# Kernel optimization log

Hardware: AMD Instinct MI355X
Metric: run time of the kernel (lower is better)

## Reference

```python
import jax, jax.numpy as jnp
import numpy as np

B, S, DIM, NH = 4, 2048, 2048, 16
HD = DIM // NH  # 128


def setup_inputs() -> dict:
    key = jax.random.key(0)
    ks = jax.random.split(key, 6)
    x = jax.random.normal(ks[0], (B, S, DIM), dtype=jnp.float32)
    wq = jax.random.normal(ks[1], (DIM, DIM), dtype=jnp.float32) * (DIM ** -0.5)
    wk = jax.random.normal(ks[2], (DIM, DIM), dtype=jnp.float32) * (DIM ** -0.5)
    wv = jax.random.normal(ks[3], (DIM, DIM), dtype=jnp.float32) * (DIM ** -0.5)
    wo = jax.random.normal(ks[4], (DIM, DIM), dtype=jnp.float32) * (DIM ** -0.5)
    # RoPE frequencies: theta^{-2i/hd}, angle = pos * freq
    inv_freq = 1.0 / (10000.0 ** (np.arange(0, HD, 2, dtype=np.float32) / HD))  # [HD/2]
    angles = np.arange(S, dtype=np.float32)[:, None] * inv_freq[None, :]  # [S, HD/2]
    freqs_cos = jnp.asarray(np.cos(angles))
    freqs_sin = jnp.asarray(np.sin(angles))
    # causal mask, additive [S, S]
    mask = jnp.where(jnp.tril(jnp.ones((S, S), dtype=bool)), 0.0, -jnp.inf).astype(jnp.float32)
    return {"x": x, "wq": wq, "wk": wk, "wv": wv, "wo": wo,
            "freqs_cos": freqs_cos, "freqs_sin": freqs_sin, "mask": mask,
            "start_pos": 0}


def _apply_rotary(xq, xk, cos, sin):
    # xq, xk: [B, S, H, HD]; cos/sin: [S, HD/2]
    def rot(t):
        tr = t.reshape(*t.shape[:-1], -1, 2)  # [B,S,H,HD/2,2]
        a, b = tr[..., 0], tr[..., 1]
        c = cos[None, :, None, :]
        s = sin[None, :, None, :]
        # complex multiply (a+ib)(c+is)
        out = jnp.stack([a * c - b * s, a * s + b * c], axis=-1)
        return out.reshape(t.shape)
    return rot(xq), rot(xk)


def reference(x, wq, wk, wv, wo, freqs_cos, freqs_sin, mask, start_pos):
    bsz, seqlen, _ = x.shape
    # nn.Linear: y = x @ W^T
    xq = (x @ wq.T).reshape(bsz, seqlen, NH, HD)
    xk = (x @ wk.T).reshape(bsz, seqlen, NH, HD)
    xv = (x @ wv.T).reshape(bsz, seqlen, NH, HD)
    xq, xk = _apply_rotary(xq, xk, freqs_cos, freqs_sin)
    # attention, heads to axis 1
    scores = jnp.einsum('bqhd,bkhd->bhqk', xq, xk) / jnp.sqrt(jnp.float32(HD))
    scores = scores + mask[None, None, :, :]
    probs = jax.nn.softmax(scores.astype(jnp.float32), axis=-1).astype(xq.dtype)
    out = jnp.einsum('bhqk,bkhd->bqhd', probs, xv).reshape(bsz, seqlen, -1)
    return out @ wo.T
```

## Files before the change

kernel.cpp:

```cpp
#include <hip/hip_runtime.h>

typedef __attribute__((ext_vector_type(8))) __bf16 bf16x8;
typedef __attribute__((ext_vector_type(4))) float f32x4;
typedef __attribute__((ext_vector_type(16))) float f32x16;
typedef __attribute__((ext_vector_type(8))) unsigned short u16x8;
typedef __attribute__((ext_vector_type(2))) unsigned uint2v;

#define LOG2E 1.44269504088896340736f

__device__ __forceinline__ unsigned short f2bf(float f){
  union { float f; unsigned u; } v; v.f = f;
  unsigned r = v.u + 0x7FFFu + ((v.u >> 16) & 1u);
  return (unsigned short)(r >> 16);
}
__device__ __forceinline__ float bf2f(unsigned short u){
  union { unsigned u; float f; } v; v.u = ((unsigned)u) << 16;
  return v.f;
}

typedef const unsigned __attribute__((address_space(1)))* gas_ptr;
typedef unsigned __attribute__((address_space(3)))* las_ptr;

__device__ __forceinline__ void gload_lds16(const void* g, void* l){
  __builtin_amdgcn_global_load_lds((gas_ptr)g, (las_ptr)l, 16, 0, 0);
}

__device__ __forceinline__ unsigned cvtpk(float lo, float hi){
  unsigned r;
  asm("v_cvt_pk_bf16_f32 %0, %1, %2" : "=v"(r) : "v"(lo), "v"(hi));
  return r;
}
__device__ __forceinline__ void swap32(unsigned &a, unsigned &b){
  uint2v r = __builtin_amdgcn_permlane32_swap(a, b, false, false);
  a = r[0]; b = r[1];
}

__global__ __launch_bounds__(256) void cvt_f32_bf16(const float* __restrict__ in,
                                                    unsigned short* __restrict__ out){
  size_t i = ((size_t)blockIdx.x * 256 + threadIdx.x) * 4;
  float4 vv = *(const float4*)(in + i);
  ushort4 o;
  o.x = f2bf(vv.x); o.y = f2bf(vv.y); o.z = f2bf(vv.z); o.w = f2bf(vv.w);
  *(ushort4*)(out + i) = o;
}

#define BUF(op, half, par) (LDS + (((op) * 2 + (half)) * 2 + (par)) * 16384)

#define STAGE(op, gbase, half, par, kt) do {                                   \
  _Pragma("unroll")                                                            \
  for (int c_ = 0; c_ < 2; ++c_){                                              \
    int slot_ = c_ * 512 + w * 64 + l;                                         \
    int row_ = slot_ >> 3, colb_ = slot_ & 7;                                  \
    gload_lds16((const char*)((gbase) + (size_t)((half) * 128 + row_) * K +    \
                              (size_t)(kt) * 64 + ((colb_ ^ (row_ & 7)) * 8)), \
                BUF(op, half, par) + c_ * 8192 + w * 1024);                    \
  } } while (0)

#define PHASE(mh, nh, par, ...) do {                                           \
  bf16x8 af_[4][2], bf_[2][2];                                                 \
  const char* Ab_ = BUF(0, mh, par);                                           \
  const char* Bb_ = BUF(1, nh, par);                                           \
  _Pragma("unroll")                                                            \
  for (int i_ = 0; i_ < 4; ++i_){                                              \
    int row_ = wm * 64 + i_ * 16 + lq;                                         \
    _Pragma("unroll")                                                          \
    for (int ks_ = 0; ks_ < 2; ++ks_)                                          \
      af_[i_][ks_] = *(const bf16x8*)(Ab_ + row_ * 128 +                       \
                                      (((ks_ * 4 + lg) ^ (row_ & 7)) * 16));   \
  }                                                                            \
  _Pragma("unroll")                                                            \
  for (int j_ = 0; j_ < 2; ++j_){                                              \
    int row_ = wn * 32 + j_ * 16 + lq;                                         \
    _Pragma("unroll")                                                          \
    for (int ks_ = 0; ks_ < 2; ++ks_)                                          \
      bf_[j_][ks_] = *(const bf16x8*)(Bb_ + row_ * 128 +                       \
                                      (((ks_ * 4 + lg) ^ (row_ & 7)) * 16));   \
  }                                                                            \
  __VA_ARGS__;                                                                 \
  __builtin_amdgcn_s_barrier();                                                \
  asm volatile("s_waitcnt lgkmcnt(0)");                                        \
  __builtin_amdgcn_s_setprio(1);                                               \
  _Pragma("unroll")                                                            \
  for (int i_ = 0; i_ < 4; ++i_)                                               \
    _Pragma("unroll")                                                          \
    for (int j_ = 0; j_ < 2; ++j_)                                             \
      _Pragma("unroll")                                                        \
      for (int ks_ = 0; ks_ < 2; ++ks_)                                        \
        acc[(mh) * 4 + i_][(nh) * 2 + j_] = __builtin_amdgcn_mfma_f32_16x16x32_bf16( \
            af_[i_][ks_], bf_[j_][ks_], acc[(mh) * 4 + i_][(nh) * 2 + j_], 0, 0, 0); \
  __builtin_amdgcn_s_setprio(0);                                               \
  __builtin_amdgcn_s_barrier();                                                \
} while (0)

template<bool OUT_BF16>
__global__ __launch_bounds__(512, 2) void gemm256(const unsigned short* __restrict__ A,
                                                  const unsigned short* __restrict__ B,
                                                  void* __restrict__ Cv,
                                                  int M, int N, int K){
  __shared__ char LDS[131072];
  const int tid = threadIdx.x;
  const int l = tid & 63, w = tid >> 6;
  const int lq = l & 15, lg = l >> 4;
  const int wm = w >> 2, wn = w & 3;

  const int nwg = gridDim.x, cpx = nwg >> 3;
  const int orig = blockIdx.x;
  const int sw = (orig & 7) * cpx + (orig >> 3);
  const int nbc = N >> 8;
  const int br = sw / nbc, bc = sw % nbc;

  f32x4 acc[8][4] = {};
  const unsigned short* Ag = A + (size_t)br * 256 * K;
  const unsigned short* Bg = B + (size_t)bc * 256 * K;
  const int NT = K >> 6;

  STAGE(0, Ag, 0, 0, 0); STAGE(1, Bg, 0, 0, 0);
  STAGE(0, Ag, 1, 0, 0); STAGE(1, Bg, 1, 0, 0);
  STAGE(1, Bg, 0, 1, 1); STAGE(0, Ag, 0, 1, 1);
  asm volatile("s_waitcnt vmcnt(4)" ::: "memory");
  __builtin_amdgcn_s_barrier();

  for (int t = 0; t < NT; ++t){
    const int par = t & 1, parn = par ^ 1;
    PHASE(0, 0, par, { if (t + 1 < NT) STAGE(0, Ag, 1, parn, t + 1); });
    PHASE(1, 0, par, { if (t + 1 < NT) STAGE(1, Bg, 1, parn, t + 1); });
    PHASE(0, 1, par, { if (t + 2 < NT) STAGE(1, Bg, 0, par, t + 2); });
    PHASE(1, 1, par, { if (t + 2 < NT) STAGE(0, Ag, 0, par, t + 2); });
    asm volatile("s_waitcnt vmcnt(4)" ::: "memory");
    __builtin_amdgcn_s_barrier();
  }

#pragma unroll
  for (int i = 0; i < 8; ++i){
    int grow = br * 256 + (i >> 2) * 128 + wm * 64 + (i & 3) * 16 + lg * 4;
#pragma unroll
    for (int j = 0; j < 4; ++j){
      int gcol = bc * 256 + (j >> 1) * 128 + wn * 32 + (j & 1) * 16 + lq;
#pragma unroll
      for (int r = 0; r < 4; ++r){
        if (OUT_BF16)
          ((unsigned short*)Cv)[(size_t)(grow + r) * N + gcol] = f2bf(acc[i][j][r]);
        else
          ((float*)Cv)[(size_t)(grow + r) * N + gcol] = acc[i][j][r];
      }
    }
  }
}

__global__ __launch_bounds__(256) void rope_kernel(unsigned short* __restrict__ q,
                                                   unsigned short* __restrict__ k,
                                                   const float* __restrict__ fc,
                                                   const float* __restrict__ fs){
  int tid = blockIdx.x * 256 + threadIdx.x;
  int col8 = tid & 255;
  int row = tid >> 8;
  int s = row & 2047;
  int i0 = (col8 & 15) * 4;
  size_t eo = (size_t)row * 2048 + (size_t)(col8 >> 4) * 128 + (size_t)(col8 & 15) * 8;
  float4 c = *(const float4*)(fc + (size_t)s * 64 + i0);
  float4 sn = *(const float4*)(fs + (size_t)s * 64 + i0);
  float cs[4] = {c.x, c.y, c.z, c.w};
  float ss[4] = {sn.x, sn.y, sn.z, sn.w};
  u16x8 qv = *(const u16x8*)(q + eo);
  u16x8 kv = *(const u16x8*)(k + eo);
  u16x8 qo, ko;
#pragma unroll
  for (int p2 = 0; p2 < 4; ++p2){
    float a = bf2f(qv[2 * p2]), b = bf2f(qv[2 * p2 + 1]);
    qo[2 * p2]     = f2bf(a * cs[p2] - b * ss[p2]);
    qo[2 * p2 + 1] = f2bf(a * ss[p2] + b * cs[p2]);
    a = bf2f(kv[2 * p2]); b = bf2f(kv[2 * p2 + 1]);
    ko[2 * p2]     = f2bf(a * cs[p2] - b * ss[p2]);
    ko[2 * p2 + 1] = f2bf(a * ss[p2] + b * cs[p2]);
  }
  *(u16x8*)(q + eo) = qo;
  *(u16x8*)(k + eo) = ko;
}

__global__ __launch_bounds__(512, 2) void attn_fwd(const unsigned short* __restrict__ Q,
                                                   const unsigned short* __restrict__ K,
                                                   const unsigned short* __restrict__ V,
                                                   unsigned short* __restrict__ O){
  __shared__ unsigned short SMEM[2 * 64 * 128 + 2 * 128 * 64];
  unsigned short* Ks = SMEM;
  unsigned short* Vt = SMEM + 16384;

  const int tid = threadIdx.x;
  const int l = tid & 63, wid = tid >> 6;
  const int lq = l & 31, hi = l >> 5;
  const int bh = blockIdx.x & 63;
  const int qt = 7 - (blockIdx.x >> 6);
  const int b = bh >> 4, h = bh & 15;
  const int qw = qt * 256 + wid * 32;
  const float c2 = 0.12751743f;

  const unsigned short* qptr = Q + ((size_t)(b * 2048 + qw + lq)) * 2048 + (size_t)h * 128;
  bf16x8 qf[8];
#pragma unroll
  for (int ks = 0; ks < 8; ++ks)
    qf[ks] = *(const bf16x8*)(qptr + ks * 16 + hi * 8);

  f32x16 oacc[4];
#pragma unroll
  for (int i = 0; i < 4; ++i)
#pragma unroll
    for (int j = 0; j < 16; ++j) oacc[i][j] = 0.f;
  float mrow = -3.0e38f, lrow = 0.f;

  const int dblk = tid >> 5, kvp = tid & 31;
  const size_t hb = (size_t)b * 2048 * 2048 + (size_t)h * 128;
  u16x8 r0, r1;

  {
    const size_t kvb = hb;
#pragma unroll
    for (int c = 0; c < 2; ++c){
      int off = c * 8192 + tid * 16;
      int row = off >> 8, colb = off & 255;
      gload_lds16((const char*)(K + kvb + (size_t)row * 2048) + (colb ^ ((row & 15) << 4)),
                  (char*)Ks + c * 8192 + (tid >> 6) * 1024 + (tid & 63) * 16);
    }
    const unsigned short* vp = V + kvb + (size_t)(2 * kvp) * 2048 + dblk * 8;
    r0 = *(const u16x8*)vp; r1 = *(const u16x8*)(vp + 2048);
    asm volatile("s_waitcnt vmcnt(0)" ::: "memory");
#pragma unroll
    for (int j = 0; j < 8; ++j){
      int d = dblk * 8 + j;
      unsigned val = (unsigned)r0[j] | ((unsigned)r1[j] << 16);
      *(unsigned*)((char*)Vt + d * 128 + ((4 * kvp) ^ ((d & 7) << 4))) = val;
    }
  }
  __syncthreads();

  const int nkt = 4 * qt + 4;
  for (int kt = 0; kt < nkt; ++kt){
    const int cur = kt & 1, nxt = cur ^ 1;
    const bool pref = (kt + 1 < nkt);
    char* KsC = (char*)(Ks + cur * 8192);
    char* VtC = (char*)(Vt + cur * 8192);

    if (pref){
      const size_t kvb = hb + (size_t)((kt + 1) * 64) * 2048;
      char* KsN = (char*)(Ks + nxt * 8192);
#pragma unroll
      for (int c = 0; c < 2; ++c){
        int off = c * 8192 + tid * 16;
        int row = off >> 8, colb = off & 255;
        gload_lds16((const char*)(K + kvb + (size_t)row * 2048) + (colb ^ ((row & 15) << 4)),
                    KsN + c * 8192 + (tid >> 6) * 1024 + (tid & 63) * 16);
      }
      const unsigned short* vp = V + kvb + (size_t)(2 * kvp) * 2048 + dblk * 8;
      r0 = *(const u16x8*)vp; r1 = *(const u16x8*)(vp + 2048);
    }

    if (!(kt * 64 > qw + 31)){
      f32x16 sacc[2];
#pragma unroll
      for (int sub = 0; sub < 2; ++sub){
#pragma unroll
        for (int j = 0; j < 16; ++j) sacc[sub][j] = 0.f;
        const int row = sub * 32 + lq;
        const int swz = (row & 15) << 4;
#pragma unroll
        for (int ks = 0; ks < 8; ++ks){
          bf16x8 kf = *(const bf16x8*)(KsC + row * 256 + ((ks * 32 + hi * 16) ^ swz));
          sacc[sub] = __builtin_amdgcn_mfma_f32_32x32x16_bf16(kf, qf[ks], sacc[sub], 0, 0, 0);
        }
      }

      float s[32];
#pragma unroll
      for (int sub = 0; sub < 2; ++sub)
#pragma unroll
        for (int r = 0; r < 16; ++r) s[sub * 16 + r] = sacc[sub][r];

      if (kt * 64 + 63 > qw){
        const int qg = qw + lq;
#pragma unroll
        for (int sub = 0; sub < 2; ++sub)
#pragma unroll
          for (int r = 0; r < 16; ++r){
            int kvg = kt * 64 + sub * 32 + (r & 3) + 8 * (r >> 2) + 4 * hi;
            if (kvg > qg) s[sub * 16 + r] = -3.0e38f;
          }
      }

      float mx[32];
#pragma unroll
      for (int i = 0; i < 32; ++i) mx[i] = s[i];
#pragma unroll
      for (int st = 1; st < 32; st <<= 1)
#pragma unroll
        for (int i = 0; i < 32; i += 2 * st) mx[i] = fmaxf(mx[i], mx[i + st]);
      float pmax = mx[0];
      pmax = fmaxf(pmax, __shfl_xor(pmax, 32, 64));

      float mm;
      if (__all((pmax - mrow) * c2 <= 8.0f)){
        mm = mrow * c2;
      } else {
        float mnew = fmaxf(mrow, pmax);
        mm = mnew * c2;
        float corr = __builtin_amdgcn_exp2f(__builtin_fmaf(mrow, c2, -mm));
        mrow = mnew;
        lrow *= corr;
#pragma unroll
        for (int i = 0; i < 4; ++i)
#pragma unroll
          for (int j = 0; j < 16; ++j) oacc[i][j] *= corr;
      }

      float p[32];
#pragma unroll
      for (int i = 0; i < 32; ++i)
        p[i] = __builtin_amdgcn_exp2f(__builtin_fmaf(s[i], c2, -mm));
      float sm[32];
#pragma unroll
      for (int i = 0; i < 32; ++i) sm[i] = p[i];
#pragma unroll
      for (int st = 1; st < 32; st <<= 1)
#pragma unroll
        for (int i = 0; i < 32; i += 2 * st) sm[i] += sm[i + st];
      float rs = sm[0];
      rs += __shfl_xor(rs, 32, 64);
      lrow += rs;

      unsigned wv[16];
#pragma unroll
      for (int i = 0; i < 16; ++i) wv[i] = cvtpk(p[2 * i], p[2 * i + 1]);
      swap32(wv[0], wv[2]);   swap32(wv[1], wv[3]);
      swap32(wv[4], wv[6]);   swap32(wv[5], wv[7]);
      swap32(wv[8], wv[10]);  swap32(wv[9], wv[11]);
      swap32(wv[12], wv[14]); swap32(wv[13], wv[15]);

#pragma unroll
      for (int c = 0; c < 4; ++c){
        union { unsigned u[4]; bf16x8 v; } pu;
        pu.u[0] = wv[c * 4 + 0]; pu.u[1] = wv[c * 4 + 1];
        pu.u[2] = wv[c * 4 + 2]; pu.u[3] = wv[c * 4 + 3];
#pragma unroll
        for (int db = 0; db < 4; ++db){
          const int d = db * 32 + lq;
          bf16x8 vf = *(const bf16x8*)(VtC + d * 128 + ((c * 32 + hi * 16) ^ ((d & 7) << 4)));
          oacc[db] = __builtin_amdgcn_mfma_f32_32x32x16_bf16(vf, pu.v, oacc[db], 0, 0, 0);
        }
      }
    }

    if (pref){
      asm volatile("s_waitcnt vmcnt(0)" ::: "memory");
      char* VtN = (char*)(Vt + nxt * 8192);
#pragma unroll
      for (int j = 0; j < 8; ++j){
        int d = dblk * 8 + j;
        unsigned val = (unsigned)r0[j] | ((unsigned)r1[j] << 16);
        *(unsigned*)(VtN + d * 128 + ((4 * kvp) ^ ((d & 7) << 4))) = val;
      }
    }
    __syncthreads();
  }

  float inv = 1.0f / lrow;
  char* lb = (char*)SMEM + wid * 8192;
#pragma unroll
  for (int db = 0; db < 4; ++db)
#pragma unroll
    for (int r = 0; r < 16; r += 2){
      int d = db * 32 + (r & 3) + 8 * (r >> 2) + 4 * hi;
      unsigned val = (unsigned)f2bf(oacc[db][r] * inv) |
                     ((unsigned)f2bf(oacc[db][r + 1] * inv) << 16);
      *(unsigned*)(lb + lq * 256 + ((2 * d) ^ ((lq & 7) << 4))) = val;
    }
  __syncthreads();
#pragma unroll
  for (int i = 0; i < 8; ++i){
    int rowq = i * 4 + (l >> 4);
    u16x8 vv = *(const u16x8*)(lb + rowq * 256 + (((l & 15) * 16) ^ ((rowq & 7) << 4)));
    *(u16x8*)(O + ((size_t)(b * 2048 + qw + rowq)) * 2048 + (size_t)h * 128 + (l & 15) * 8) = vv;
  }
}

extern "C" void kernel_launch(void* const* d_in, const int* in_sizes, int n_in,
                              void* d_out, int out_size, void* d_ws, size_t ws_size,
                              hipStream_t stream){
  const float* x  = (const float*)d_in[0];
  const float* wq = (const float*)d_in[1];
  const float* wk = (const float*)d_in[2];
  const float* wv = (const float*)d_in[3];
  const float* wo = (const float*)d_in[4];
  const float* fc = (const float*)d_in[5];
  const float* fs = (const float*)d_in[6];
  float* out = (float*)d_out;
  (void)in_sizes; (void)n_in; (void)out_size; (void)ws_size;

  const size_t XN = (size_t)8192 * 2048;
  const size_t WN = (size_t)2048 * 2048;

  unsigned short* xb  = (unsigned short*)d_ws;
  unsigned short* wqb = xb + XN;
  unsigned short* wkb = wqb + WN;
  unsigned short* wvb = wkb + WN;
  unsigned short* wob = wvb + WN;
  unsigned short* q   = wob + WN;
  unsigned short* k   = q + XN;
  unsigned short* v   = k + XN;
  unsigned short* att = xb;

  cvt_f32_bf16<<<dim3((unsigned)(XN / 1024)), 256, 0, stream>>>(x, xb);
  cvt_f32_bf16<<<dim3((unsigned)(WN / 1024)), 256, 0, stream>>>(wq, wqb);
  cvt_f32_bf16<<<dim3((unsigned)(WN / 1024)), 256, 0, stream>>>(wk, wkb);
  cvt_f32_bf16<<<dim3((unsigned)(WN / 1024)), 256, 0, stream>>>(wv, wvb);
  cvt_f32_bf16<<<dim3((unsigned)(WN / 1024)), 256, 0, stream>>>(wo, wob);

  gemm256<true><<<dim3(256), 512, 0, stream>>>(xb, wqb, q, 8192, 2048, 2048);
  gemm256<true><<<dim3(256), 512, 0, stream>>>(xb, wkb, k, 8192, 2048, 2048);
  gemm256<true><<<dim3(256), 512, 0, stream>>>(xb, wvb, v, 8192, 2048, 2048);

  rope_kernel<<<dim3(8192), 256, 0, stream>>>(q, k, fc, fs);

  attn_fwd<<<dim3(512), 512, 0, stream>>>(q, k, v, att);

  gemm256<false><<<dim3(256), 512, 0, stream>>>(att, wob, out, 8192, 2048, 2048);
}
```

Before: 449.2 us.

## Fuse RoPE into QK GEMM epilogue and pair causal query tiles per block

```diff
diff --git a/kernel.cpp b/kernel.cpp
--- a/kernel.cpp
+++ b/kernel.cpp
@@ -92,11 +92,13 @@
   __builtin_amdgcn_s_barrier();                                                \
 } while (0)
 
-template<bool OUT_BF16>
+template<bool OUT_BF16, bool ROPE>
 __global__ __launch_bounds__(512, 2) void gemm256(const unsigned short* __restrict__ A,
                                                   const unsigned short* __restrict__ B,
                                                   void* __restrict__ Cv,
-                                                  int M, int N, int K){
+                                                  int M, int N, int K,
+                                                  const float* __restrict__ fc,
+                                                  const float* __restrict__ fs){
   __shared__ char LDS[131072];
   const int tid = threadIdx.x;
   const int l = tid & 63, w = tid >> 6;
@@ -138,43 +140,22 @@
       int gcol = bc * 256 + (j >> 1) * 128 + wn * 32 + (j & 1) * 16 + lq;
 #pragma unroll
       for (int r = 0; r < 4; ++r){
+        float v = acc[i][j][r];
+        if (ROPE){
+          int s = (grow + r) & 2047;
+          int i0 = (gcol & 127) >> 1;
+          float cc = fc[s * 64 + i0], sn = fs[s * 64 + i0];
+          float part = __shfl_xor(v, 1, 64);
+          v = (lq & 1) ? __builtin_fmaf(part, sn, v * cc)
+                       : __builtin_fmaf(-part, sn, v * cc);
+        }
         if (OUT_BF16)
-          ((unsigned short*)Cv)[(size_t)(grow + r) * N + gcol] = f2bf(acc[i][j][r]);
+          ((unsigned short*)Cv)[(size_t)(grow + r) * N + gcol] = f2bf(v);
         else
-          ((float*)Cv)[(size_t)(grow + r) * N + gcol] = acc[i][j][r];
+          ((float*)Cv)[(size_t)(grow + r) * N + gcol] = v;
       }
     }
   }
-}
-
-__global__ __launch_bounds__(256) void rope_kernel(unsigned short* __restrict__ q,
-                                                   unsigned short* __restrict__ k,
-                                                   const float* __restrict__ fc,
-                                                   const float* __restrict__ fs){
-  int tid = blockIdx.x * 256 + threadIdx.x;
-  int col8 = tid & 255;
-  int row = tid >> 8;
-  int s = row & 2047;
-  int i0 = (col8 & 15) * 4;
-  size_t eo = (size_t)row * 2048 + (size_t)(col8 >> 4) * 128 + (size_t)(col8 & 15) * 8;
-  float4 c = *(const float4*)(fc + (size_t)s * 64 + i0);
-  float4 sn = *(const float4*)(fs + (size_t)s * 64 + i0);
-  float cs[4] = {c.x, c.y, c.z, c.w};
-  float ss[4] = {sn.x, sn.y, sn.z, sn.w};
-  u16x8 qv = *(const u16x8*)(q + eo);
-  u16x8 kv = *(const u16x8*)(k + eo);
-  u16x8 qo, ko;
-#pragma unroll
-  for (int p2 = 0; p2 < 4; ++p2){
-    float a = bf2f(qv[2 * p2]), b = bf2f(qv[2 * p2 + 1]);
-    qo[2 * p2]     = f2bf(a * cs[p2] - b * ss[p2]);
-    qo[2 * p2 + 1] = f2bf(a * ss[p2] + b * cs[p2]);
-    a = bf2f(kv[2 * p2]); b = bf2f(kv[2 * p2 + 1]);
-    ko[2 * p2]     = f2bf(a * cs[p2] - b * ss[p2]);
-    ko[2 * p2 + 1] = f2bf(a * ss[p2] + b * cs[p2]);
-  }
-  *(u16x8*)(q + eo) = qo;
-  *(u16x8*)(k + eo) = ko;
 }
 
 __global__ __launch_bounds__(512, 2) void attn_fwd(const unsigned short* __restrict__ Q,
@@ -189,194 +170,199 @@
   const int l = tid & 63, wid = tid >> 6;
   const int lq = l & 31, hi = l >> 5;
   const int bh = blockIdx.x & 63;
-  const int qt = 7 - (blockIdx.x >> 6);
+  const int pair = blockIdx.x >> 6;
   const int b = bh >> 4, h = bh & 15;
-  const int qw = qt * 256 + wid * 32;
   const float c2 = 0.12751743f;
-
-  const unsigned short* qptr = Q + ((size_t)(b * 2048 + qw + lq)) * 2048 + (size_t)h * 128;
-  bf16x8 qf[8];
-#pragma unroll
-  for (int ks = 0; ks < 8; ++ks)
-    qf[ks] = *(const bf16x8*)(qptr + ks * 16 + hi * 8);
-
-  f32x16 oacc[4];
-#pragma unroll
-  for (int i = 0; i < 4; ++i)
-#pragma unroll
-    for (int j = 0; j < 16; ++j) oacc[i][j] = 0.f;
-  float mrow = -3.0e38f, lrow = 0.f;
 
   const int dblk = tid >> 5, kvp = tid & 31;
   const size_t hb = (size_t)b * 2048 * 2048 + (size_t)h * 128;
-  u16x8 r0, r1;
-
-  {
-    const size_t kvb = hb;
-#pragma unroll
-    for (int c = 0; c < 2; ++c){
-      int off = c * 8192 + tid * 16;
-      int row = off >> 8, colb = off & 255;
-      gload_lds16((const char*)(K + kvb + (size_t)row * 2048) + (colb ^ ((row & 15) << 4)),
-                  (char*)Ks + c * 8192 + (tid >> 6) * 1024 + (tid & 63) * 16);
-    }
-    const unsigned short* vp = V + kvb + (size_t)(2 * kvp) * 2048 + dblk * 8;
-    r0 = *(const u16x8*)vp; r1 = *(const u16x8*)(vp + 2048);
-    asm volatile("s_waitcnt vmcnt(0)" ::: "memory");
-#pragma unroll
-    for (int j = 0; j < 8; ++j){
-      int d = dblk * 8 + j;
-      unsigned val = (unsigned)r0[j] | ((unsigned)r1[j] << 16);
-      *(unsigned*)((char*)Vt + d * 128 + ((4 * kvp) ^ ((d & 7) << 4))) = val;
-    }
-  }
-  __syncthreads();
-
-  const int nkt = 4 * qt + 4;
-  for (int kt = 0; kt < nkt; ++kt){
-    const int cur = kt & 1, nxt = cur ^ 1;
-    const bool pref = (kt + 1 < nkt);
-    char* KsC = (char*)(Ks + cur * 8192);
-    char* VtC = (char*)(Vt + cur * 8192);
-
-    if (pref){
-      const size_t kvb = hb + (size_t)((kt + 1) * 64) * 2048;
-      char* KsN = (char*)(Ks + nxt * 8192);
+
+  for (int strip = 0; strip < 2; ++strip){
+    const int qt = strip == 0 ? pair : 7 - pair;
+    const int qw = qt * 256 + wid * 32;
+
+    const unsigned short* qptr = Q + ((size_t)(b * 2048 + qw + lq)) * 2048 + (size_t)h * 128;
+    bf16x8 qf[8];
+#pragma unroll
+    for (int ks = 0; ks < 8; ++ks)
+      qf[ks] = *(const bf16x8*)(qptr + ks * 16 + hi * 8);
+
+    f32x16 oacc[4];
+#pragma unroll
+    for (int i = 0; i < 4; ++i)
+#pragma unroll
+      for (int j = 0; j < 16; ++j) oacc[i][j] = 0.f;
+    float mrow = -3.0e38f, lrow = 0.f;
+    u16x8 r0, r1;
+
+    {
+      const size_t kvb = hb;
 #pragma unroll
       for (int c = 0; c < 2; ++c){
         int off = c * 8192 + tid * 16;
         int row = off >> 8, colb = off & 255;
         gload_lds16((const char*)(K + kvb + (size_t)row * 2048) + (colb ^ ((row & 15) << 4)),
-                    KsN + c * 8192 + (tid >> 6) * 1024 + (tid & 63) * 16);
+                    (char*)Ks + c * 8192 + (tid >> 6) * 1024 + (tid & 63) * 16);
       }
       const unsigned short* vp = V + kvb + (size_t)(2 * kvp) * 2048 + dblk * 8;
       r0 = *(const u16x8*)vp; r1 = *(const u16x8*)(vp + 2048);
-    }
-
-    if (!(kt * 64 > qw + 31)){
-      f32x16 sacc[2];
-#pragma unroll
-      for (int sub = 0; sub < 2; ++sub){
-#pragma unroll
-        for (int j = 0; j < 16; ++j) sacc[sub][j] = 0.f;
-        const int row = sub * 32 + lq;
-        const int swz = (row & 15) << 4;
-#pragma unroll
-        for (int ks = 0; ks < 8; ++ks){
-          bf16x8 kf = *(const bf16x8*)(KsC + row * 256 + ((ks * 32 + hi * 16) ^ swz));
-          sacc[sub] = __builtin_amdgcn_mfma_f32_32x32x16_bf16(kf, qf[ks], sacc[sub], 0, 0, 0);
-        }
-      }
-
-      float s[32];
-#pragma unroll
-      for (int sub = 0; sub < 2; ++sub)
-#pragma unroll
-        for (int r = 0; r < 16; ++r) s[sub * 16 + r] = sacc[sub][r];
-
-      if (kt * 64 + 63 > qw){
-        const int qg = qw + lq;
-#pragma unroll
-        for (int sub = 0; sub < 2; ++sub)
-#pragma unroll
-          for (int r = 0; r < 16; ++r){
-            int kvg = kt * 64 + sub * 32 + (r & 3) + 8 * (r >> 2) + 4 * hi;
-            if (kvg > qg) s[sub * 16 + r] = -3.0e38f;
-          }
-      }
-
-      float mx[32];
-#pragma unroll
-      for (int i = 0; i < 32; ++i) mx[i] = s[i];
-#pragma unroll
-      for (int st = 1; st < 32; st <<= 1)
-#pragma unroll
-        for (int i = 0; i < 32; i += 2 * st) mx[i] = fmaxf(mx[i], mx[i + st]);
-      float pmax = mx[0];
-      pmax = fmaxf(pmax, __shfl_xor(pmax, 32, 64));
-
-      float mm;
-      if (__all((pmax - mrow) * c2 <= 8.0f)){
-        mm = mrow * c2;
-      } else {
-        float mnew = fmaxf(mrow, pmax);
-        mm = mnew * c2;
-        float corr = __builtin_amdgcn_exp2f(__builtin_fmaf(mrow, c2, -mm));
-        mrow = mnew;
-        lrow *= corr;
-#pragma unroll
-        for (int i = 0; i < 4; ++i)
-#pragma unroll
-          for (int j = 0; j < 16; ++j) oacc[i][j] *= corr;
-      }
-
-      float p[32];
-#pragma unroll
-      for (int i = 0; i < 32; ++i)
-        p[i] = __builtin_amdgcn_exp2f(__builtin_fmaf(s[i], c2, -mm));
-      float sm[32];
-#pragma unroll
-      for (int i = 0; i < 32; ++i) sm[i] = p[i];
-#pragma unroll
-      for (int st = 1; st < 32; st <<= 1)
-#pragma unroll
-        for (int i = 0; i < 32; i += 2 * st) sm[i] += sm[i + st];
-      float rs = sm[0];
-      rs += __shfl_xor(rs, 32, 64);
-      lrow += rs;
-
-      unsigned wv[16];
-#pragma unroll
-      for (int i = 0; i < 16; ++i) wv[i] = cvtpk(p[2 * i], p[2 * i + 1]);
-      swap32(wv[0], wv[2]);   swap32(wv[1], wv[3]);
-      swap32(wv[4], wv[6]);   swap32(wv[5], wv[7]);
-      swap32(wv[8], wv[10]);  swap32(wv[9], wv[11]);
-      swap32(wv[12], wv[14]); swap32(wv[13], wv[15]);
-
-#pragma unroll
-      for (int c = 0; c < 4; ++c){
-        union { unsigned u[4]; bf16x8 v; } pu;
-        pu.u[0] = wv[c * 4 + 0]; pu.u[1] = wv[c * 4 + 1];
-        pu.u[2] = wv[c * 4 + 2]; pu.u[3] = wv[c * 4 + 3];
-#pragma unroll
-        for (int db = 0; db < 4; ++db){
-          const int d = db * 32 + lq;
-          bf16x8 vf = *(const bf16x8*)(VtC + d * 128 + ((c * 32 + hi * 16) ^ ((d & 7) << 4)));
-          oacc[db] = __builtin_amdgcn_mfma_f32_32x32x16_bf16(vf, pu.v, oacc[db], 0, 0, 0);
-        }
-      }
-    }
-
-    if (pref){
       asm volatile("s_waitcnt vmcnt(0)" ::: "memory");
-      char* VtN = (char*)(Vt + nxt * 8192);
 #pragma unroll
       for (int j = 0; j < 8; ++j){
         int d = dblk * 8 + j;
         unsigned val = (unsigned)r0[j] | ((unsigned)r1[j] << 16);
-        *(unsigned*)(VtN + d * 128 + ((4 * kvp) ^ ((d & 7) << 4))) = val;
+        *(unsigned*)((char*)Vt + d * 128 + ((4 * kvp) ^ ((d & 7) << 4))) = val;
       }
     }
     __syncthreads();
-  }
-
-  float inv = 1.0f / lrow;
-  char* lb = (char*)SMEM + wid * 8192;
-#pragma unroll
-  for (int db = 0; db < 4; ++db)
-#pragma unroll
-    for (int r = 0; r < 16; r += 2){
-      int d = db * 32 + (r & 3) + 8 * (r >> 2) + 4 * hi;
-      unsigned val = (unsigned)f2bf(oacc[db][r] * inv) |
-                     ((unsigned)f2bf(oacc[db][r + 1] * inv) << 16);
-      *(unsigned*)(lb + lq * 256 + ((2 * d) ^ ((lq & 7) << 4))) = val;
+
+    const int nkt = 4 * qt + 4;
+    for (int kt = 0; kt < nkt; ++kt){
+      const int cur = kt & 1, nxt = cur ^ 1;
+      const bool pref = (kt + 1 < nkt);
+      char* KsC = (char*)(Ks + cur * 8192);
+      char* VtC = (char*)(Vt + cur * 8192);
+
+      if (pref){
+        const size_t kvb = hb + (size_t)((kt + 1) * 64) * 2048;
+        char* KsN = (char*)(Ks + nxt * 8192);
+#pragma unroll
+        for (int c = 0; c < 2; ++c){
+          int off = c * 8192 + tid * 16;
+          int row = off >> 8, colb = off & 255;
+          gload_lds16((const char*)(K + kvb + (size_t)row * 2048) + (colb ^ ((row & 15) << 4)),
+                      KsN + c * 8192 + (tid >> 6) * 1024 + (tid & 63) * 16);
+        }
+        const unsigned short* vp = V + kvb + (size_t)(2 * kvp) * 2048 + dblk * 8;
+        r0 = *(const u16x8*)vp; r1 = *(const u16x8*)(vp + 2048);
+      }
+
+      if (!(kt * 64 > qw + 31)){
+        f32x16 sacc[2];
+#pragma unroll
+        for (int sub = 0; sub < 2; ++sub){
+#pragma unroll
+          for (int j = 0; j < 16; ++j) sacc[sub][j] = 0.f;
+          const int row = sub * 32 + lq;
+          const int swz = (row & 15) << 4;
+#pragma unroll
+          for (int ks = 0; ks < 8; ++ks){
+            bf16x8 kf = *(const bf16x8*)(KsC + row * 256 + ((ks * 32 + hi * 16) ^ swz));
+            sacc[sub] = __builtin_amdgcn_mfma_f32_32x32x16_bf16(kf, qf[ks], sacc[sub], 0, 0, 0);
+          }
+        }
+
+        float s[32];
+#pragma unroll
+        for (int sub = 0; sub < 2; ++sub)
+#pragma unroll
+          for (int r = 0; r < 16; ++r) s[sub * 16 + r] = sacc[sub][r];
+
+        if (kt * 64 + 63 > qw){
+          const int qg = qw + lq;
+#pragma unroll
+          for (int sub = 0; sub < 2; ++sub)
+#pragma unroll
+            for (int r = 0; r < 16; ++r){
+              int kvg = kt * 64 + sub * 32 + (r & 3) + 8 * (r >> 2) + 4 * hi;
+              if (kvg > qg) s[sub * 16 + r] = -3.0e38f;
+            }
+        }
+
+        float mx[32];
+#pragma unroll
+        for (int i = 0; i < 32; ++i) mx[i] = s[i];
+#pragma unroll
+        for (int st = 1; st < 32; st <<= 1)
+#pragma unroll
+          for (int i = 0; i < 32; i += 2 * st) mx[i] = fmaxf(mx[i], mx[i + st]);
+        float pmax = mx[0];
+        pmax = fmaxf(pmax, __shfl_xor(pmax, 32, 64));
+
+        float mm;
+        if (__all((pmax - mrow) * c2 <= 8.0f)){
+          mm = mrow * c2;
+        } else {
+          float mnew = fmaxf(mrow, pmax);
+          mm = mnew * c2;
+          float corr = __builtin_amdgcn_exp2f(__builtin_fmaf(mrow, c2, -mm));
+          mrow = mnew;
+          lrow *= corr;
+#pragma unroll
+          for (int i = 0; i < 4; ++i)
+#pragma unroll
+            for (int j = 0; j < 16; ++j) oacc[i][j] *= corr;
+        }
+
+        float p[32];
+#pragma unroll
+        for (int i = 0; i < 32; ++i)
+          p[i] = __builtin_amdgcn_exp2f(__builtin_fmaf(s[i], c2, -mm));
+        float sm[32];
+#pragma unroll
+        for (int i = 0; i < 32; ++i) sm[i] = p[i];
+#pragma unroll
+        for (int st = 1; st < 32; st <<= 1)
+#pragma unroll
+          for (int i = 0; i < 32; i += 2 * st) sm[i] += sm[i + st];
+        float rs = sm[0];
+        rs += __shfl_xor(rs, 32, 64);
+        lrow += rs;
+
+        unsigned wv[16];
+#pragma unroll
+        for (int i = 0; i < 16; ++i) wv[i] = cvtpk(p[2 * i], p[2 * i + 1]);
+        swap32(wv[0], wv[2]);   swap32(wv[1], wv[3]);
+        swap32(wv[4], wv[6]);   swap32(wv[5], wv[7]);
+        swap32(wv[8], wv[10]);  swap32(wv[9], wv[11]);
+        swap32(wv[12], wv[14]); swap32(wv[13], wv[15]);
+
+#pragma unroll
+        for (int c = 0; c < 4; ++c){
+          union { unsigned u[4]; bf16x8 v; } pu;
+          pu.u[0] = wv[c * 4 + 0]; pu.u[1] = wv[c * 4 + 1];
+          pu.u[2] = wv[c * 4 + 2]; pu.u[3] = wv[c * 4 + 3];
+#pragma unroll
+          for (int db = 0; db < 4; ++db){
+            const int d = db * 32 + lq;
+            bf16x8 vf = *(const bf16x8*)(VtC + d * 128 + ((c * 32 + hi * 16) ^ ((d & 7) << 4)));
+            oacc[db] = __builtin_amdgcn_mfma_f32_32x32x16_bf16(vf, pu.v, oacc[db], 0, 0, 0);
+          }
+        }
+      }
+
+      if (pref){
+        asm volatile("s_waitcnt vmcnt(0)" ::: "memory");
+        char* VtN = (char*)(Vt + nxt * 8192);
+#pragma unroll
+        for (int j = 0; j < 8; ++j){
+          int d = dblk * 8 + j;
+          unsigned val = (unsigned)r0[j] | ((unsigned)r1[j] << 16);
+          *(unsigned*)(VtN + d * 128 + ((4 * kvp) ^ ((d & 7) << 4))) = val;
+        }
+      }
+      __syncthreads();
     }
-  __syncthreads();
-#pragma unroll
-  for (int i = 0; i < 8; ++i){
-    int rowq = i * 4 + (l >> 4);
-    u16x8 vv = *(const u16x8*)(lb + rowq * 256 + (((l & 15) * 16) ^ ((rowq & 7) << 4)));
-    *(u16x8*)(O + ((size_t)(b * 2048 + qw + rowq)) * 2048 + (size_t)h * 128 + (l & 15) * 8) = vv;
+
+    float inv = 1.0f / lrow;
+    char* lb = (char*)SMEM + wid * 8192;
+#pragma unroll
+    for (int db = 0; db < 4; ++db)
+#pragma unroll
+      for (int r = 0; r < 16; r += 2){
+        int d = db * 32 + (r & 3) + 8 * (r >> 2) + 4 * hi;
+        unsigned val = (unsigned)f2bf(oacc[db][r] * inv) |
+                       ((unsigned)f2bf(oacc[db][r + 1] * inv) << 16);
+        *(unsigned*)(lb + lq * 256 + ((2 * d) ^ ((lq & 7) << 4))) = val;
+      }
+    __syncthreads();
+#pragma unroll
+    for (int i = 0; i < 8; ++i){
+      int rowq = i * 4 + (l >> 4);
+      u16x8 vv = *(const u16x8*)(lb + rowq * 256 + (((l & 15) * 16) ^ ((rowq & 7) << 4)));
+      *(u16x8*)(O + ((size_t)(b * 2048 + qw + rowq)) * 2048 + (size_t)h * 128 + (l & 15) * 8) = vv;
+    }
+    __syncthreads();
   }
 }
 
@@ -412,13 +398,11 @@
   cvt_f32_bf16<<<dim3((unsigned)(WN / 1024)), 256, 0, stream>>>(wv, wvb);
   cvt_f32_bf16<<<dim3((unsigned)(WN / 1024)), 256, 0, stream>>>(wo, wob);
 
-  gemm256<true><<<dim3(256), 512, 0, stream>>>(xb, wqb, q, 8192, 2048, 2048);
-  gemm256<true><<<dim3(256), 512, 0, stream>>>(xb, wkb, k, 8192, 2048, 2048);
-  gemm256<true><<<dim3(256), 512, 0, stream>>>(xb, wvb, v, 8192, 2048, 2048);
-
-  rope_kernel<<<dim3(8192), 256, 0, stream>>>(q, k, fc, fs);
-
-  attn_fwd<<<dim3(512), 512, 0, stream>>>(q, k, v, att);
-
-  gemm256<false><<<dim3(256), 512, 0, stream>>>(att, wob, out, 8192, 2048, 2048);
-}
+  gemm256<true, true ><<<dim3(256), 512, 0, stream>>>(xb, wqb, q, 8192, 2048, 2048, fc, fs);
+  gemm256<true, true ><<<dim3(256), 512, 0, stream>>>(xb, wkb, k, 8192, 2048, 2048, fc, fs);
+  gemm256<true, false><<<dim3(256), 512, 0, stream>>>(xb, wvb, v, 8192, 2048, 2048, nullptr, nullptr);
+
+  attn_fwd<<<dim3(256), 512, 0, stream>>>(q, k, v, att);
+
+  gemm256<false, false><<<dim3(256), 512, 0, stream>>>(att, wob, out, 8192, 2048, 2048, nullptr, nullptr);
+}
```

New measurement: 463.5 us. 3.2% more time.
